# Optimization experiments

Hardware: AMD Instinct MI355X
Metric: run time of the kernel (lower is better)

Reference implementation:

```python
import jax, jax.numpy as jnp
import numpy as np
import math

B, S, D, H = 2, 2048, 1024, 16

def setup_inputs() -> dict:
    key = jax.random.key(0)
    ks = jax.random.split(key, 13)
    def lin(kw, kb, out_d, in_d):
        W = jax.random.normal(kw, (out_d, in_d), dtype=jnp.float32) * 0.02
        b = jax.random.normal(kb, (out_d,), dtype=jnp.float32) * 0.02
        return W, b
    Wq, bq = lin(ks[0], ks[1], D, D)
    Wk, bk = lin(ks[2], ks[3], D, D)
    Wv, bv = lin(ks[4], ks[5], D, D)
    Wo, bo = lin(ks[6], ks[7], D, D)
    query = jax.random.normal(ks[8], (B, S, D), dtype=jnp.float32)
    key_t = jax.random.normal(ks[9], (B, S, D), dtype=jnp.float32)
    value = jax.random.normal(ks[10], (B, S, D), dtype=jnp.float32)
    src_mask = jax.random.randint(ks[11], (B, S), 0, 2).astype(bool)  # True = masked out
    return {"query": query, "key": key_t, "value": value, "src_mask": src_mask,
            "Wq": Wq, "bq": bq, "Wk": Wk, "bk": bk, "Wv": Wv, "bv": bv,
            "Wo": Wo, "bo": bo, "nhead": H}

def reference(query, key, value, src_mask, Wq, bq, Wk, bk, Wv, bv, Wo, bo, nhead):
    b, s, d = query.shape
    hd = d // nhead
    scale = 1.0 / math.sqrt(hd)
    def split_heads(x):  # [b,s,d] -> [b,h,s,hd]
        return x.reshape(b, -1, nhead, hd).transpose(0, 2, 1, 3)
    q = split_heads(query @ Wq.T + bq)
    k = split_heads(key @ Wk.T + bk)
    v = split_heads(value @ Wv.T + bv)
    scores = jnp.einsum('bhqe,bhke->bhqk', q, k) * scale  # [b,h,s,s]
    # mask True -> -9e9, broadcast over heads and query positions (matches repeat)
    scores = jnp.where(src_mask[:, None, None, :], jnp.float32(-9e9), scores)
    probs = jax.nn.softmax(scores, axis=-1)
    # dropout is identity in eval mode
    out = jnp.einsum('bhqk,bhke->bhqe', probs, v)  # [b,h,s,hd]
    out = out.transpose(0, 2, 1, 3).reshape(b, s, d)
    out = out @ Wo.T + bo
    return out
```

## Files before the change

### kernel.cpp

```cpp
#include <hip/hip_runtime.h>
#include <hip/hip_bf16.h>
#include <cstdint>
#include <cstddef>

#define B_ 2
#define S_ 2048
#define D_ 1024
#define H_ 16
#define HD_ 64
#define M_ 4096

typedef __attribute__((ext_vector_type(8))) short short8;
typedef __attribute__((ext_vector_type(4))) float floatx4;

__device__ __forceinline__ floatx4 mfma16(short8 a, short8 b, floatx4 c) {
    return __builtin_amdgcn_mfma_f32_16x16x32_bf16(a, b, c, 0, 0, 0);
}

__device__ __forceinline__ void gload_lds16(const __hip_bfloat16* g, __hip_bfloat16* lds_base) {
    __builtin_amdgcn_global_load_lds(
        (const __attribute__((address_space(1))) void*)g,
        (__attribute__((address_space(3))) void*)lds_base, 16, 0, 0);
}

__global__ __launch_bounds__(256) void cvt3_kernel(
    const float* __restrict__ a, const float* __restrict__ b, const float* __restrict__ c,
    __hip_bfloat16* __restrict__ dst, int n)
{
    const float* src = blockIdx.z == 0 ? a : blockIdx.z == 1 ? b : c;
    __hip_bfloat16* d = dst + (size_t)blockIdx.z * n;
    int i = (blockIdx.x * 256 + threadIdx.x) * 4;
    float4 v = *(const float4*)(src + i);
    union { __hip_bfloat16 h[4]; uint2 u; } cv;
    cv.h[0] = __float2bfloat16(v.x); cv.h[1] = __float2bfloat16(v.y);
    cv.h[2] = __float2bfloat16(v.z); cv.h[3] = __float2bfloat16(v.w);
    *(uint2*)(d + i) = cv.u;
}

__global__ __launch_bounds__(256) void cvt4_kernel(
    const float* __restrict__ a, const float* __restrict__ b,
    const float* __restrict__ c, const float* __restrict__ e,
    __hip_bfloat16* __restrict__ dst, int n)
{
    const float* src = blockIdx.z == 0 ? a : blockIdx.z == 1 ? b : blockIdx.z == 2 ? c : e;
    __hip_bfloat16* d = dst + (size_t)blockIdx.z * n;
    int i = (blockIdx.x * 256 + threadIdx.x) * 4;
    float4 v = *(const float4*)(src + i);
    union { __hip_bfloat16 h[4]; uint2 u; } cv;
    cv.h[0] = __float2bfloat16(v.x); cv.h[1] = __float2bfloat16(v.y);
    cv.h[2] = __float2bfloat16(v.z); cv.h[3] = __float2bfloat16(v.w);
    *(uint2*)(d + i) = cv.u;
}

template <int MODE>
__device__ __forceinline__ void gemm_core(
    const __hip_bfloat16* __restrict__ A,
    const __hip_bfloat16* __restrict__ W,
    const float* __restrict__ bias,
    void* __restrict__ Cout,
    __hip_bfloat16* __restrict__ smem,
    int m0, int n0, int N)
{
    __hip_bfloat16* As = smem;
    __hip_bfloat16* Bs = smem + 128 * 32;
    const int K = D_;
    const int tid  = threadIdx.x;
    const int wave = tid >> 6;
    const int lane = tid & 63;
    const int quad = lane >> 4;
    const int l15  = lane & 15;
    const int wm   = (wave & 1) * 64;
    const int wn   = (wave >> 1) * 64;
    const int srow = lane >> 2;
    const int scol = (lane & 3) * 8;

    floatx4 acc[4][4];
#pragma unroll
    for (int i = 0; i < 4; i++)
#pragma unroll
        for (int j = 0; j < 4; j++) {
            floatx4 z = {0.f, 0.f, 0.f, 0.f};
            acc[i][j] = z;
        }

    for (int k0 = 0; k0 < K; k0 += 32) {
        __syncthreads();
#pragma unroll
        for (int t = 0; t < 2; t++) {
            int r0 = wave * 32 + t * 16;
            gload_lds16(A + (size_t)(m0 + r0 + srow) * K + k0 + scol, As + r0 * 32);
            gload_lds16(W + (size_t)(n0 + r0 + srow) * K + k0 + scol, Bs + r0 * 32);
        }
        __syncthreads();

        short8 afr[4], bfr[4];
#pragma unroll
        for (int i = 0; i < 4; i++)
            afr[i] = *(const short8*)(As + (wm + i * 16 + l15) * 32 + quad * 8);
#pragma unroll
        for (int j = 0; j < 4; j++)
            bfr[j] = *(const short8*)(Bs + (wn + j * 16 + l15) * 32 + quad * 8);
#pragma unroll
        for (int i = 0; i < 4; i++)
#pragma unroll
            for (int j = 0; j < 4; j++)
                acc[i][j] = mfma16(afr[i], bfr[j], acc[i][j]);
    }

#pragma unroll
    for (int j = 0; j < 4; j++) {
        int col = n0 + wn + j * 16 + l15;
        float bv = bias[col];
#pragma unroll
        for (int i = 0; i < 4; i++) {
#pragma unroll
            for (int r = 0; r < 4; r++) {
                int rowg = m0 + wm + i * 16 + quad * 4 + r;
                float val = acc[i][j][r] + bv;
                if constexpr (MODE == 0) {
                    ((__hip_bfloat16*)Cout)[(size_t)rowg * N + col] = __float2bfloat16(val);
                } else if constexpr (MODE == 1) {
                    int h = col >> 6, e = col & 63;
                    int b = rowg >> 11, s = rowg & 2047;
                    ((__hip_bfloat16*)Cout)[(((size_t)b * H_ + h) * HD_ + e) * S_ + s] =
                        __float2bfloat16(val);
                } else {
                    ((float*)Cout)[(size_t)rowg * N + col] = val;
                }
            }
        }
    }
}

__global__ __launch_bounds__(256) void qkv_gemm_kernel(
    const __hip_bfloat16* __restrict__ qb, const __hip_bfloat16* __restrict__ kb,
    const __hip_bfloat16* __restrict__ vb,
    const __hip_bfloat16* __restrict__ Wqb, const __hip_bfloat16* __restrict__ Wkb,
    const __hip_bfloat16* __restrict__ Wvb,
    const float* __restrict__ bq, const float* __restrict__ bk, const float* __restrict__ bv,
    __hip_bfloat16* __restrict__ Qp, __hip_bfloat16* __restrict__ Kp,
    __hip_bfloat16* __restrict__ Vt)
{
    __shared__ __hip_bfloat16 smem[2 * 128 * 32] __attribute__((aligned(16)));
    const int z = blockIdx.z;
    const __hip_bfloat16* A = z == 0 ? qb : z == 1 ? kb : vb;
    const __hip_bfloat16* W = z == 0 ? Wqb : z == 1 ? Wkb : Wvb;
    const float* bias = z == 0 ? bq : z == 1 ? bk : bv;
    int m0 = blockIdx.y * 128, n0 = blockIdx.x * 128;
    if (z < 2) gemm_core<0>(A, W, bias, z == 0 ? (void*)Qp : (void*)Kp, smem, m0, n0, D_);
    else       gemm_core<1>(A, W, bias, (void*)Vt, smem, m0, n0, D_);
}

__global__ __launch_bounds__(256) void oproj_gemm_kernel(
    const __hip_bfloat16* __restrict__ A, const __hip_bfloat16* __restrict__ Wob,
    const float* __restrict__ bo, float* __restrict__ out)
{
    __shared__ __hip_bfloat16 smem[2 * 128 * 32] __attribute__((aligned(16)));
    gemm_core<2>(A, Wob, bo, (void*)out, smem, blockIdx.y * 128, blockIdx.x * 128, D_);
}

#define LDP 72
__global__ __launch_bounds__(256) void flash_attn_kernel(
    const __hip_bfloat16* __restrict__ Q,
    const __hip_bfloat16* __restrict__ Kp,
    const __hip_bfloat16* __restrict__ Vt,
    const int* __restrict__ mask,
    __hip_bfloat16* __restrict__ O)
{
    __shared__ __hip_bfloat16 Qs [64 * LDP] __attribute__((aligned(16)));
    __shared__ __hip_bfloat16 Ks [64 * LDP] __attribute__((aligned(16)));
    __shared__ __hip_bfloat16 Vts[64 * LDP] __attribute__((aligned(16)));
    __shared__ __hip_bfloat16 Ps [64 * LDP] __attribute__((aligned(16)));

    const int tid  = threadIdx.x;
    const int q0   = blockIdx.x * 64;
    const int bh   = blockIdx.y;
    const int b    = bh >> 4;
    const int h    = bh & 15;
    const int wave = tid >> 6;
    const int lane = tid & 63;
    const int quad = lane >> 4;
    const int l15  = lane & 15;
    const float scale = 0.125f;

    const size_t baseQ = ((size_t)b * S_ + q0) * D_ + (size_t)h * HD_;
#pragma unroll
    for (int c = tid; c < 512; c += 256) {
        int row = c >> 3, kc = c & 7;
        *(uint4*)(Qs + row * LDP + kc * 8) = *(const uint4*)(Q + baseQ + (size_t)row * D_ + kc * 8);
    }
    __syncthreads();

    short8 qa[2];
    qa[0] = *(const short8*)(Qs + (wave * 16 + l15) * LDP + quad * 8);
    qa[1] = *(const short8*)(Qs + (wave * 16 + l15) * LDP + 32 + quad * 8);

    float l_part[4] = {0.f, 0.f, 0.f, 0.f};
    floatx4 o_acc[4];
#pragma unroll
    for (int ot = 0; ot < 4; ot++) {
        floatx4 z = {0.f, 0.f, 0.f, 0.f};
        o_acc[ot] = z;
    }

    const int* mrow = mask + b * S_;
    const __hip_bfloat16* VtBase = Vt + (size_t)bh * HD_ * S_;

    for (int kv0 = 0; kv0 < S_; kv0 += 64) {
        __syncthreads();
        const size_t baseK = ((size_t)b * S_ + kv0) * D_ + (size_t)h * HD_;
#pragma unroll
        for (int c = tid; c < 512; c += 256) {
            int row = c >> 3, kc = c & 7;
            *(uint4*)(Ks + row * LDP + kc * 8) =
                *(const uint4*)(Kp + baseK + (size_t)row * D_ + kc * 8);
            *(uint4*)(Vts + row * LDP + kc * 8) =
                *(const uint4*)(VtBase + (size_t)row * S_ + kv0 + kc * 8);
        }
        __syncthreads();

        floatx4 s_acc[4];
#pragma unroll
        for (int nt = 0; nt < 4; nt++) {
            short8 kb0 = *(const short8*)(Ks + (nt * 16 + l15) * LDP + quad * 8);
            short8 kb1 = *(const short8*)(Ks + (nt * 16 + l15) * LDP + 32 + quad * 8);
            floatx4 z = {0.f, 0.f, 0.f, 0.f};
            z = mfma16(qa[0], kb0, z);
            z = mfma16(qa[1], kb1, z);
            s_acc[nt] = z;
        }

#pragma unroll
        for (int nt = 0; nt < 4; nt++) {
            bool msk = (mrow[kv0 + nt * 16 + l15] != 0);
#pragma unroll
            for (int r = 0; r < 4; r++) {
                float pe = msk ? 0.f : __expf(s_acc[nt][r] * scale);
                s_acc[nt][r] = pe;
                l_part[r] += pe;
                Ps[(wave * 16 + quad * 4 + r) * LDP + nt * 16 + l15] = __float2bfloat16(pe);
            }
        }

#pragma unroll
        for (int ks = 0; ks < 2; ks++) {
            short8 pa = *(const short8*)(Ps + (wave * 16 + l15) * LDP + ks * 32 + quad * 8);
#pragma unroll
            for (int ot = 0; ot < 4; ot++) {
                short8 vb = *(const short8*)(Vts + (ot * 16 + l15) * LDP + ks * 32 + quad * 8);
                o_acc[ot] = mfma16(pa, vb, o_acc[ot]);
            }
        }
    }

#pragma unroll
    for (int off = 1; off < 16; off <<= 1)
#pragma unroll
        for (int r = 0; r < 4; r++)
            l_part[r] += __shfl_xor(l_part[r], off);

    const size_t baseO = ((size_t)b * S_ + q0) * D_ + (size_t)h * HD_;
#pragma unroll
    for (int r = 0; r < 4; r++) {
        float inv = 1.0f / l_part[r];
        int rowl = wave * 16 + quad * 4 + r;
#pragma unroll
        for (int ot = 0; ot < 4; ot++) {
            O[baseO + (size_t)rowl * D_ + ot * 16 + l15] =
                __float2bfloat16(o_acc[ot][r] * inv);
        }
    }
}

extern "C" void kernel_launch(void* const* d_in, const int* in_sizes, int n_in,
                              void* d_out, int out_size, void* d_ws, size_t ws_size,
                              hipStream_t stream) {
    const float* query = (const float*)d_in[0];
    const float* key   = (const float*)d_in[1];
    const float* value = (const float*)d_in[2];
    const int*   mask  = (const int*)d_in[3];
    const float* Wq    = (const float*)d_in[4];
    const float* bq    = (const float*)d_in[5];
    const float* Wk    = (const float*)d_in[6];
    const float* bk    = (const float*)d_in[7];
    const float* Wv    = (const float*)d_in[8];
    const float* bv    = (const float*)d_in[9];
    const float* Wo    = (const float*)d_in[10];
    const float* bo    = (const float*)d_in[11];
    float* out = (float*)d_out;

    const size_t SZ_IN = (size_t)M_ * D_;
    const size_t SZ_W  = (size_t)D_ * D_;
    __hip_bfloat16* qb  = (__hip_bfloat16*)d_ws;
    __hip_bfloat16* kb  = qb  + SZ_IN;
    __hip_bfloat16* vb  = kb  + SZ_IN;
    __hip_bfloat16* Wqb = vb  + SZ_IN;
    __hip_bfloat16* Wkb = Wqb + SZ_W;
    __hip_bfloat16* Wvb = Wkb + SZ_W;
    __hip_bfloat16* Wob = Wvb + SZ_W;
    __hip_bfloat16* Qp  = Wob + SZ_W;
    __hip_bfloat16* Kp  = Qp  + SZ_IN;
    __hip_bfloat16* Vt  = Kp  + SZ_IN;

    cvt3_kernel<<<dim3(SZ_IN / 1024, 1, 3), 256, 0, stream>>>(query, key, value, qb, (int)SZ_IN);
    cvt4_kernel<<<dim3(SZ_W / 1024, 1, 4), 256, 0, stream>>>(Wq, Wk, Wv, Wo, Wqb, (int)SZ_W);

    qkv_gemm_kernel<<<dim3(D_ / 128, M_ / 128, 3), 256, 0, stream>>>(
        qb, kb, vb, Wqb, Wkb, Wvb, bq, bk, bv, Qp, Kp, Vt);

    flash_attn_kernel<<<dim3(S_ / 64, B_ * H_), 256, 0, stream>>>(Qp, Kp, Vt, mask, Qp);

    oproj_gemm_kernel<<<dim3(D_ / 128, M_ / 128), 256, 0, stream>>>(Qp, Wob, bo, out);
}
```

Baseline: 257.8 us.

## Keep softmax probabilities in registers and double query rows per attention block

The attention kernel now computes S^T by swapping the MFMA operands, so each lane holds P values in the layout that a 16x16x16 MFMA accepts as its A operand. This removes the LDS round trip for P. Each block now handles 128 query rows (32 per wave), so each K/V tile load is reused across twice as many queries. The kernel also uses exp2 with a folded scale, loads the mask as vectors, and in the QKV GEMM writes the transposed V output as packed 4-element stores. The trade-off is fewer blocks (half the grid) and higher register pressure from the doubled accumulators.

```diff
diff --git a/kernel.cpp b/kernel.cpp
--- a/kernel.cpp
+++ b/kernel.cpp
@@ -11,10 +11,14 @@
 #define M_ 4096
 
 typedef __attribute__((ext_vector_type(8))) short short8;
+typedef __attribute__((ext_vector_type(4))) short shortx4;
 typedef __attribute__((ext_vector_type(4))) float floatx4;
 
-__device__ __forceinline__ floatx4 mfma16(short8 a, short8 b, floatx4 c) {
+__device__ __forceinline__ floatx4 mfma32(short8 a, short8 b, floatx4 c) {
     return __builtin_amdgcn_mfma_f32_16x16x32_bf16(a, b, c, 0, 0, 0);
+}
+__device__ __forceinline__ floatx4 mfma16(shortx4 a, shortx4 b, floatx4 c) {
+    return __builtin_amdgcn_mfma_f32_16x16x16bf16_1k(a, b, c, 0, 0, 0);
 }
 
 __device__ __forceinline__ void gload_lds16(const __hip_bfloat16* g, __hip_bfloat16* lds_base) {
@@ -104,28 +108,41 @@
         for (int i = 0; i < 4; i++)
 #pragma unroll
             for (int j = 0; j < 4; j++)
-                acc[i][j] = mfma16(afr[i], bfr[j], acc[i][j]);
-    }
-
-#pragma unroll
-    for (int j = 0; j < 4; j++) {
-        int col = n0 + wn + j * 16 + l15;
-        float bv = bias[col];
-#pragma unroll
-        for (int i = 0; i < 4; i++) {
-#pragma unroll
-            for (int r = 0; r < 4; r++) {
-                int rowg = m0 + wm + i * 16 + quad * 4 + r;
-                float val = acc[i][j][r] + bv;
-                if constexpr (MODE == 0) {
-                    ((__hip_bfloat16*)Cout)[(size_t)rowg * N + col] = __float2bfloat16(val);
-                } else if constexpr (MODE == 1) {
-                    int h = col >> 6, e = col & 63;
-                    int b = rowg >> 11, s = rowg & 2047;
-                    ((__hip_bfloat16*)Cout)[(((size_t)b * H_ + h) * HD_ + e) * S_ + s] =
-                        __float2bfloat16(val);
-                } else {
-                    ((float*)Cout)[(size_t)rowg * N + col] = val;
+                acc[i][j] = mfma32(afr[i], bfr[j], acc[i][j]);
+    }
+
+    if constexpr (MODE == 1) {
+#pragma unroll
+        for (int j = 0; j < 4; j++) {
+            int col = n0 + wn + j * 16 + l15;
+            int h = col >> 6, e = col & 63;
+            float bv = bias[col];
+#pragma unroll
+            for (int i = 0; i < 4; i++) {
+                int s0 = m0 + wm + i * 16 + quad * 4;
+                int bb = s0 >> 11, sl = s0 & 2047;
+                union { __hip_bfloat16 hx[4]; uint2 u; } pk;
+#pragma unroll
+                for (int r = 0; r < 4; r++)
+                    pk.hx[r] = __float2bfloat16(acc[i][j][r] + bv);
+                *(uint2*)((__hip_bfloat16*)Cout + (((size_t)bb * H_ + h) * HD_ + e) * S_ + sl) = pk.u;
+            }
+        }
+    } else {
+#pragma unroll
+        for (int j = 0; j < 4; j++) {
+            int col = n0 + wn + j * 16 + l15;
+            float bv = bias[col];
+#pragma unroll
+            for (int i = 0; i < 4; i++) {
+#pragma unroll
+                for (int r = 0; r < 4; r++) {
+                    int rowg = m0 + wm + i * 16 + quad * 4 + r;
+                    float val = acc[i][j][r] + bv;
+                    if constexpr (MODE == 0)
+                        ((__hip_bfloat16*)Cout)[(size_t)rowg * N + col] = __float2bfloat16(val);
+                    else
+                        ((float*)Cout)[(size_t)rowg * N + col] = val;
                 }
             }
         }
@@ -167,13 +184,12 @@
     const int* __restrict__ mask,
     __hip_bfloat16* __restrict__ O)
 {
-    __shared__ __hip_bfloat16 Qs [64 * LDP] __attribute__((aligned(16)));
-    __shared__ __hip_bfloat16 Ks [64 * LDP] __attribute__((aligned(16)));
-    __shared__ __hip_bfloat16 Vts[64 * LDP] __attribute__((aligned(16)));
-    __shared__ __hip_bfloat16 Ps [64 * LDP] __attribute__((aligned(16)));
+    __shared__ __hip_bfloat16 Qs [128 * LDP] __attribute__((aligned(16)));
+    __shared__ __hip_bfloat16 Ks [64 * LDP]  __attribute__((aligned(16)));
+    __shared__ __hip_bfloat16 Vts[64 * LDP]  __attribute__((aligned(16)));
 
     const int tid  = threadIdx.x;
-    const int q0   = blockIdx.x * 64;
+    const int q0   = blockIdx.x * 128;
     const int bh   = blockIdx.y;
     const int b    = bh >> 4;
     const int h    = bh & 15;
@@ -181,27 +197,32 @@
     const int lane = tid & 63;
     const int quad = lane >> 4;
     const int l15  = lane & 15;
-    const float scale = 0.125f;
+    const float kSc = 0.18033688f;
 
     const size_t baseQ = ((size_t)b * S_ + q0) * D_ + (size_t)h * HD_;
 #pragma unroll
-    for (int c = tid; c < 512; c += 256) {
+    for (int c = tid; c < 1024; c += 256) {
         int row = c >> 3, kc = c & 7;
         *(uint4*)(Qs + row * LDP + kc * 8) = *(const uint4*)(Q + baseQ + (size_t)row * D_ + kc * 8);
     }
     __syncthreads();
 
-    short8 qa[2];
-    qa[0] = *(const short8*)(Qs + (wave * 16 + l15) * LDP + quad * 8);
-    qa[1] = *(const short8*)(Qs + (wave * 16 + l15) * LDP + 32 + quad * 8);
-
-    float l_part[4] = {0.f, 0.f, 0.f, 0.f};
-    floatx4 o_acc[4];
-#pragma unroll
-    for (int ot = 0; ot < 4; ot++) {
-        floatx4 z = {0.f, 0.f, 0.f, 0.f};
-        o_acc[ot] = z;
-    }
+    short8 qb[2][2];
+#pragma unroll
+    for (int qt = 0; qt < 2; qt++)
+#pragma unroll
+        for (int h2 = 0; h2 < 2; h2++)
+            qb[qt][h2] = *(const short8*)(Qs + (wave * 32 + qt * 16 + l15) * LDP + h2 * 32 + quad * 8);
+
+    float lsum[2] = {0.f, 0.f};
+    floatx4 o_acc[2][4];
+#pragma unroll
+    for (int qt = 0; qt < 2; qt++)
+#pragma unroll
+        for (int ot = 0; ot < 4; ot++) {
+            floatx4 z = {0.f, 0.f, 0.f, 0.f};
+            o_acc[qt][ot] = z;
+        }
 
     const int* mrow = mask + b * S_;
     const __hip_bfloat16* VtBase = Vt + (size_t)bh * HD_ * S_;
@@ -219,55 +240,71 @@
         }
         __syncthreads();
 
-        floatx4 s_acc[4];
+        int4 mq[4];
+#pragma unroll
+        for (int nt = 0; nt < 4; nt++)
+            mq[nt] = *(const int4*)(mrow + kv0 + nt * 16 + quad * 4);
+
+        floatx4 s_acc[2][4];
 #pragma unroll
         for (int nt = 0; nt < 4; nt++) {
             short8 kb0 = *(const short8*)(Ks + (nt * 16 + l15) * LDP + quad * 8);
             short8 kb1 = *(const short8*)(Ks + (nt * 16 + l15) * LDP + 32 + quad * 8);
-            floatx4 z = {0.f, 0.f, 0.f, 0.f};
-            z = mfma16(qa[0], kb0, z);
-            z = mfma16(qa[1], kb1, z);
-            s_acc[nt] = z;
+#pragma unroll
+            for (int qt = 0; qt < 2; qt++) {
+                floatx4 z = {0.f, 0.f, 0.f, 0.f};
+                z = mfma32(kb0, qb[qt][0], z);
+                z = mfma32(kb1, qb[qt][1], z);
+                s_acc[qt][nt] = z;
+            }
+        }
+
+        shortx4 pf[2][4];
+#pragma unroll
+        for (int qt = 0; qt < 2; qt++) {
+#pragma unroll
+            for (int nt = 0; nt < 4; nt++) {
+                float pe0 = mq[nt].x ? 0.f : __builtin_amdgcn_exp2f(s_acc[qt][nt][0] * kSc);
+                float pe1 = mq[nt].y ? 0.f : __builtin_amdgcn_exp2f(s_acc[qt][nt][1] * kSc);
+                float pe2 = mq[nt].z ? 0.f : __builtin_amdgcn_exp2f(s_acc[qt][nt][2] * kSc);
+                float pe3 = mq[nt].w ? 0.f : __builtin_amdgcn_exp2f(s_acc[qt][nt][3] * kSc);
+                lsum[qt] += (pe0 + pe1) + (pe2 + pe3);
+                union { shortx4 s4; __hip_bfloat162 b2[2]; } pk;
+                pk.b2[0] = __float22bfloat162_rn({pe0, pe1});
+                pk.b2[1] = __float22bfloat162_rn({pe2, pe3});
+                pf[qt][nt] = pk.s4;
+            }
         }
 
 #pragma unroll
         for (int nt = 0; nt < 4; nt++) {
-            bool msk = (mrow[kv0 + nt * 16 + l15] != 0);
-#pragma unroll
-            for (int r = 0; r < 4; r++) {
-                float pe = msk ? 0.f : __expf(s_acc[nt][r] * scale);
-                s_acc[nt][r] = pe;
-                l_part[r] += pe;
-                Ps[(wave * 16 + quad * 4 + r) * LDP + nt * 16 + l15] = __float2bfloat16(pe);
-            }
-        }
-
-#pragma unroll
-        for (int ks = 0; ks < 2; ks++) {
-            short8 pa = *(const short8*)(Ps + (wave * 16 + l15) * LDP + ks * 32 + quad * 8);
 #pragma unroll
             for (int ot = 0; ot < 4; ot++) {
-                short8 vb = *(const short8*)(Vts + (ot * 16 + l15) * LDP + ks * 32 + quad * 8);
-                o_acc[ot] = mfma16(pa, vb, o_acc[ot]);
-            }
-        }
-    }
-
-#pragma unroll
-    for (int off = 1; off < 16; off <<= 1)
-#pragma unroll
-        for (int r = 0; r < 4; r++)
-            l_part[r] += __shfl_xor(l_part[r], off);
+                shortx4 vb = *(const shortx4*)(Vts + (ot * 16 + l15) * LDP + nt * 16 + quad * 4);
+#pragma unroll
+                for (int qt = 0; qt < 2; qt++)
+                    o_acc[qt][ot] = mfma16(pf[qt][nt], vb, o_acc[qt][ot]);
+            }
+        }
+    }
+
+#pragma unroll
+    for (int qt = 0; qt < 2; qt++) {
+        lsum[qt] += __shfl_xor(lsum[qt], 16);
+        lsum[qt] += __shfl_xor(lsum[qt], 32);
+    }
 
     const size_t baseO = ((size_t)b * S_ + q0) * D_ + (size_t)h * HD_;
 #pragma unroll
-    for (int r = 0; r < 4; r++) {
-        float inv = 1.0f / l_part[r];
-        int rowl = wave * 16 + quad * 4 + r;
-#pragma unroll
-        for (int ot = 0; ot < 4; ot++) {
-            O[baseO + (size_t)rowl * D_ + ot * 16 + l15] =
-                __float2bfloat16(o_acc[ot][r] * inv);
+    for (int qt = 0; qt < 2; qt++) {
+#pragma unroll
+        for (int r = 0; r < 4; r++) {
+            float inv = 1.0f / __shfl(lsum[qt], quad * 4 + r);
+            int rowl = wave * 32 + qt * 16 + quad * 4 + r;
+#pragma unroll
+            for (int ot = 0; ot < 4; ot++)
+                O[baseO + (size_t)rowl * D_ + ot * 16 + l15] =
+                    __float2bfloat16(o_acc[qt][ot][r] * inv);
         }
     }
 }
@@ -308,7 +345,7 @@
     qkv_gemm_kernel<<<dim3(D_ / 128, M_ / 128, 3), 256, 0, stream>>>(
         qb, kb, vb, Wqb, Wkb, Wvb, bq, bk, bv, Qp, Kp, Vt);
 
-    flash_attn_kernel<<<dim3(S_ / 64, B_ * H_), 256, 0, stream>>>(Qp, Kp, Vt, mask, Qp);
+    flash_attn_kernel<<<dim3(S_ / 128, B_ * H_), 256, 0, stream>>>(Qp, Kp, Vt, mask, Qp);
 
     oproj_gemm_kernel<<<dim3(D_ / 128, M_ / 128), 256, 0, stream>>>(Qp, Wob, bo, out);
 }
```

Result: faster. 251.5 us (-2.4%).
